# Optimization experiments

Hardware: AMD Instinct MI355X
Metric: run time of the kernel (lower is better)

Reference implementation:

```python
import jax, jax.numpy as jnp
import numpy as np

N = 1_000_000
C = 128
G = 1024  # num graphs (segments)


def setup_inputs() -> dict:
    key = jax.random.key(0)
    k1, k2, k3 = jax.random.split(key, 3)
    x = jax.random.normal(k1, (N, C), dtype=jnp.float32)
    W = jax.random.normal(k2, (C, 1), dtype=jnp.float32) / np.sqrt(C)
    b = jnp.zeros((1,), dtype=jnp.float32)
    batch = jnp.sort(jax.random.randint(k3, (N,), 0, G, dtype=jnp.int64))
    return {"x": x, "W": W, "b": b, "batch": batch}


def reference(x, W, b, batch):
    # att_lin(x): [N, 1]; softmax over dim 0 (GLOBAL over all nodes, per torch code)
    logits = x @ W + b                       # [N, 1]
    alpha = jax.nn.softmax(logits, axis=0)   # [N, 1]
    # per-graph weighted sum: replaces the Python loop with one O(N) segment-sum
    pooled = jax.ops.segment_sum(alpha * x, batch, num_segments=G)  # [G, C]
    return pooled, alpha
```

## Files before the change

kernel.cpp:

```cpp
#include <hip/hip_runtime.h>

#define C_CH 128
#define G_SEGS 1024

__global__ __launch_bounds__(256) void nap_main(
    const float* __restrict__ x, const float* __restrict__ W,
    const float* __restrict__ b, const int* __restrict__ batch,
    float* __restrict__ U, float* __restrict__ Z,
    float* __restrict__ e_out, int N)
{
    const int tid = blockIdx.x * blockDim.x + threadIdx.x;
    const int hw  = tid >> 5;
    const int sub = threadIdx.x & 31;
    const int nhw = (gridDim.x * blockDim.x) >> 5;
    const int chunk = (N + nhw - 1) / nhw;
    const int row0 = hw * chunk;
    const int row1 = min(N, row0 + chunk);

    const float4 w4 = ((const float4*)W)[sub];
    const float bv = b[0];

    float4 acc = make_float4(0.f, 0.f, 0.f, 0.f);
    int cur = -1;
    float zloc = 0.f;

    for (int row = row0; row < row1; ++row) {
        const float4 xv = ((const float4*)(x + (size_t)row * C_CH))[sub];
        float d = xv.x * w4.x + xv.y * w4.y + xv.z * w4.z + xv.w * w4.w;
        d += __shfl_xor(d, 1);
        d += __shfl_xor(d, 2);
        d += __shfl_xor(d, 4);
        d += __shfl_xor(d, 8);
        d += __shfl_xor(d, 16);
        const float e = __expf(d + bv);
        const int seg = batch[row];
        if (seg != cur) {
            if (cur >= 0) {
                float* dst = U + (size_t)cur * C_CH + sub * 4;
                atomicAdd(dst + 0, acc.x);
                atomicAdd(dst + 1, acc.y);
                atomicAdd(dst + 2, acc.z);
                atomicAdd(dst + 3, acc.w);
            }
            cur = seg;
            acc = make_float4(0.f, 0.f, 0.f, 0.f);
        }
        acc.x += e * xv.x;
        acc.y += e * xv.y;
        acc.z += e * xv.z;
        acc.w += e * xv.w;
        if (sub == 0) {
            zloc += e;
            e_out[row] = e;
        }
    }
    if (cur >= 0) {
        float* dst = U + (size_t)cur * C_CH + sub * 4;
        atomicAdd(dst + 0, acc.x);
        atomicAdd(dst + 1, acc.y);
        atomicAdd(dst + 2, acc.z);
        atomicAdd(dst + 3, acc.w);
    }
    if (sub == 0 && row0 < row1) atomicAdd(Z, zloc);
}

__global__ __launch_bounds__(256) void nap_finalize(
    const float* __restrict__ U, const float* __restrict__ Z,
    float* __restrict__ pooled, float* __restrict__ alpha,
    int gc, int n)
{
    const float inv = 1.0f / (*Z);
    const int tid = blockIdx.x * blockDim.x + threadIdx.x;
    const int stride = gridDim.x * blockDim.x;
    const int gc4 = gc >> 2;
    const int n4 = n >> 2;
    for (int k = tid; k < gc4; k += stride) {
        float4 u = ((const float4*)U)[k];
        u.x *= inv; u.y *= inv; u.z *= inv; u.w *= inv;
        ((float4*)pooled)[k] = u;
    }
    for (int k = tid; k < n4; k += stride) {
        float4 e = ((const float4*)alpha)[k];
        e.x *= inv; e.y *= inv; e.z *= inv; e.w *= inv;
        ((float4*)alpha)[k] = e;
    }
    for (int k = gc4 * 4 + tid; k < gc; k += stride) pooled[k] = U[k] * inv;
    for (int k = n4 * 4 + tid; k < n; k += stride) alpha[k] = alpha[k] * inv;
}

extern "C" void kernel_launch(void* const* d_in, const int* in_sizes, int n_in,
                              void* d_out, int out_size, void* d_ws, size_t ws_size,
                              hipStream_t stream) {
    const float* x     = (const float*)d_in[0];
    const float* W     = (const float*)d_in[1];
    const float* b     = (const float*)d_in[2];
    const int*   batch = (const int*)d_in[3];
    const int N = in_sizes[3];

    float* U = (float*)d_ws;
    float* Z = U + (size_t)G_SEGS * C_CH;
    float* pooled = (float*)d_out;
    float* alpha  = pooled + (size_t)G_SEGS * C_CH;

    hipMemsetAsync(d_ws, 0, ((size_t)G_SEGS * C_CH + 1) * sizeof(float), stream);

    nap_main<<<2048, 256, 0, stream>>>(x, W, b, batch, U, Z, alpha, N);
    nap_finalize<<<512, 256, 0, stream>>>(U, Z, pooled, alpha, G_SEGS * C_CH, N);
}
```

Baseline: 762.2 us.

## Process 8 rows per wave iteration with 64-lane full-wave loads

Restructures the main kernel so that each 64-lane wave handles eight rows per iteration, each half-wave owning alternate rows, with four float4 loads in flight per lane. This gives more memory-level parallelism and uses the whole wave instead of the former 32-lane groups. A fast path skips per-row segment checks when the whole 8-row block belongs to one segment. Alpha values are written as vectorized float4 stores, and the Z partial sums are reduced per block before a single atomic. In exchange the code becomes more complex, and the segment-boundary path now issues extra batch loads and splits flushes across the two half-waves.

After: 675.1 us. 11.4% less time.

```diff
diff --git a/kernel.cpp b/kernel.cpp
--- a/kernel.cpp
+++ b/kernel.cpp
@@ -2,6 +2,16 @@
 
 #define C_CH 128
 #define G_SEGS 1024
+
+__device__ __forceinline__ void flush_acc(float* __restrict__ U, int seg, int col4,
+                                          float4& acc) {
+    float* dst = U + (size_t)seg * C_CH + col4 * 4;
+    atomicAdd(dst + 0, acc.x);
+    atomicAdd(dst + 1, acc.y);
+    atomicAdd(dst + 2, acc.z);
+    atomicAdd(dst + 3, acc.w);
+    acc = make_float4(0.f, 0.f, 0.f, 0.f);
+}
 
 __global__ __launch_bounds__(256) void nap_main(
     const float* __restrict__ x, const float* __restrict__ W,
@@ -9,59 +19,111 @@
     float* __restrict__ U, float* __restrict__ Z,
     float* __restrict__ e_out, int N)
 {
-    const int tid = blockIdx.x * blockDim.x + threadIdx.x;
-    const int hw  = tid >> 5;
-    const int sub = threadIdx.x & 31;
-    const int nhw = (gridDim.x * blockDim.x) >> 5;
-    const int chunk = (N + nhw - 1) / nhw;
-    const int row0 = hw * chunk;
+    __shared__ float zred[4];
+    const int lane = threadIdx.x & 63;
+    const int wid  = threadIdx.x >> 6;
+    const int wave = (blockIdx.x * blockDim.x + threadIdx.x) >> 6;
+    const int nwaves = (gridDim.x * blockDim.x) >> 6;
+    int chunk = (N + nwaves - 1) / nwaves;
+    chunk = (chunk + 7) & ~7;
+    const int row0 = wave * chunk;
     const int row1 = min(N, row0 + chunk);
 
-    const float4 w4 = ((const float4*)W)[sub];
+    const int col4 = lane & 31;
+    const int h    = lane >> 5;
+    const float4 w4 = ((const float4*)W)[col4];
     const float bv = b[0];
+    const float4* x4 = (const float4*)x;
 
     float4 acc = make_float4(0.f, 0.f, 0.f, 0.f);
+    float zloc = 0.f;
     int cur = -1;
-    float zloc = 0.f;
 
-    for (int row = row0; row < row1; ++row) {
-        const float4 xv = ((const float4*)(x + (size_t)row * C_CH))[sub];
-        float d = xv.x * w4.x + xv.y * w4.y + xv.z * w4.z + xv.w * w4.w;
-        d += __shfl_xor(d, 1);
-        d += __shfl_xor(d, 2);
-        d += __shfl_xor(d, 4);
-        d += __shfl_xor(d, 8);
-        d += __shfl_xor(d, 16);
-        const float e = __expf(d + bv);
-        const int seg = batch[row];
-        if (seg != cur) {
-            if (cur >= 0) {
-                float* dst = U + (size_t)cur * C_CH + sub * 4;
-                atomicAdd(dst + 0, acc.x);
-                atomicAdd(dst + 1, acc.y);
-                atomicAdd(dst + 2, acc.z);
-                atomicAdd(dst + 3, acc.w);
+    int rb = row0;
+    for (; rb + 8 <= row1; rb += 8) {
+        const float4* p = x4 + (size_t)rb * (C_CH / 4);
+        float4 a0 = p[lane];
+        float4 a1 = p[64  + lane];
+        float4 a2 = p[128 + lane];
+        float4 a3 = p[192 + lane];
+        const int bfirst = batch[rb];
+        const int blast  = batch[rb + 7];
+
+        float d0 = a0.x * w4.x + a0.y * w4.y + a0.z * w4.z + a0.w * w4.w;
+        float d1 = a1.x * w4.x + a1.y * w4.y + a1.z * w4.z + a1.w * w4.w;
+        float d2 = a2.x * w4.x + a2.y * w4.y + a2.z * w4.z + a2.w * w4.w;
+        float d3 = a3.x * w4.x + a3.y * w4.y + a3.z * w4.z + a3.w * w4.w;
+        #pragma unroll
+        for (int m = 1; m <= 16; m <<= 1) {
+            d0 += __shfl_xor(d0, m);
+            d1 += __shfl_xor(d1, m);
+            d2 += __shfl_xor(d2, m);
+            d3 += __shfl_xor(d3, m);
+        }
+        const float e0 = __expf(d0 + bv);
+        const float e1 = __expf(d1 + bv);
+        const float e2 = __expf(d2 + bv);
+        const float e3 = __expf(d3 + bv);
+
+        if (bfirst == blast) {
+            if (bfirst != cur) {
+                if (cur >= 0) flush_acc(U, cur, col4, acc);
+                cur = bfirst;
             }
-            cur = seg;
-            acc = make_float4(0.f, 0.f, 0.f, 0.f);
+            acc.x += e0 * a0.x + e1 * a1.x + e2 * a2.x + e3 * a3.x;
+            acc.y += e0 * a0.y + e1 * a1.y + e2 * a2.y + e3 * a3.y;
+            acc.z += e0 * a0.z + e1 * a1.z + e2 * a2.z + e3 * a3.z;
+            acc.w += e0 * a0.w + e1 * a1.w + e2 * a2.w + e3 * a3.w;
+        } else {
+            const int r  = rb + h;
+            const int s0 = batch[r];
+            const int s1 = batch[r + 2];
+            const int s2 = batch[r + 4];
+            const int s3 = batch[r + 6];
+            if (s0 != cur) { if (cur >= 0) flush_acc(U, cur, col4, acc); cur = s0; }
+            acc.x += e0 * a0.x; acc.y += e0 * a0.y; acc.z += e0 * a0.z; acc.w += e0 * a0.w;
+            if (s1 != cur) { flush_acc(U, cur, col4, acc); cur = s1; }
+            acc.x += e1 * a1.x; acc.y += e1 * a1.y; acc.z += e1 * a1.z; acc.w += e1 * a1.w;
+            if (s2 != cur) { flush_acc(U, cur, col4, acc); cur = s2; }
+            acc.x += e2 * a2.x; acc.y += e2 * a2.y; acc.z += e2 * a2.z; acc.w += e2 * a2.w;
+            if (s3 != cur) { flush_acc(U, cur, col4, acc); cur = s3; }
+            acc.x += e3 * a3.x; acc.y += e3 * a3.y; acc.z += e3 * a3.z; acc.w += e3 * a3.w;
         }
-        acc.x += e * xv.x;
-        acc.y += e * xv.y;
-        acc.z += e * xv.z;
-        acc.w += e * xv.w;
-        if (sub == 0) {
-            zloc += e;
-            e_out[row] = e;
+
+        const float p0 = __shfl_xor(e0, 32);
+        const float p1 = __shfl_xor(e1, 32);
+        const float p2 = __shfl_xor(e2, 32);
+        const float p3 = __shfl_xor(e3, 32);
+        if (lane == 0) {
+            ((float4*)(e_out + rb))[0] = make_float4(e0, p0, e1, p1);
+            zloc += e0 + e1 + e2 + e3;
+        } else if (lane == 32) {
+            ((float4*)(e_out + rb))[1] = make_float4(p2, e2, p3, e3);
+            zloc += e0 + e1 + e2 + e3;
         }
     }
-    if (cur >= 0) {
-        float* dst = U + (size_t)cur * C_CH + sub * 4;
-        atomicAdd(dst + 0, acc.x);
-        atomicAdd(dst + 1, acc.y);
-        atomicAdd(dst + 2, acc.z);
-        atomicAdd(dst + 3, acc.w);
+
+    for (; rb < row1; ++rb) {
+        const float4 xv = x4[(size_t)rb * (C_CH / 4) + col4];
+        float d = xv.x * w4.x + xv.y * w4.y + xv.z * w4.z + xv.w * w4.w;
+        #pragma unroll
+        for (int m = 1; m <= 16; m <<= 1) d += __shfl_xor(d, m);
+        const float e = __expf(d + bv);
+        const int s = batch[rb];
+        if (h == 0) {
+            if (s != cur) { if (cur >= 0) flush_acc(U, cur, col4, acc); cur = s; }
+            acc.x += e * xv.x; acc.y += e * xv.y; acc.z += e * xv.z; acc.w += e * xv.w;
+            if (lane == 0) { e_out[rb] = e; zloc += e; }
+        }
     }
-    if (sub == 0 && row0 < row1) atomicAdd(Z, zloc);
+
+    if (cur >= 0) flush_acc(U, cur, col4, acc);
+
+    zloc += __shfl_xor(zloc, 32);
+    if (lane == 0) zred[wid] = zloc;
+    __syncthreads();
+    if (threadIdx.x == 0)
+        atomicAdd(Z, zred[0] + zred[1] + zred[2] + zred[3]);
 }
 
 __global__ __launch_bounds__(256) void nap_finalize(
```
